# Kernel tuning notes

Measured on AMD Instinct MI355X. Metric: run time of the kernel, lower is better.

The kernel has to match this reference:

```python
import jax, jax.numpy as jnp
import numpy as np


def _build_kkt(A, B, x0, C, c, T):
    n_state, n_ctrl = B.shape
    n_all = n_state + n_ctrl
    N = n_all * T          # primal dim (z)
    M = n_state * T        # dual dim (mu)
    dt = A.dtype

    # TL = block_diag(C_0, ..., C_{T-1})  -> [N, N]
    t = jnp.arange(T)
    ra = jnp.arange(n_all)
    rows = t[:, None, None] * n_all + ra[None, :, None]
    cols = t[:, None, None] * n_all + ra[None, None, :]
    TL = jnp.zeros((N, N), dt).at[rows, cols].set(C)

    # BL = dynamics constraint matrix  -> [M, N]
    AB = jnp.concatenate([A, B], axis=1)            # [n_state, n_all]
    BL = jnp.zeros((M, N), dt)
    BL = BL.at[:n_state, :n_state].set(jnp.eye(n_state, dtype=dt))
    ti = jnp.arange(T - 1)
    rs = jnp.arange(n_state)
    # AB blocks: rows n_state + i*n_state, cols i*n_all (i = 0..T-2)
    br = (ti[:, None, None] + 1) * n_state + rs[None, :, None]
    bc = ti[:, None, None] * n_all + ra[None, None, :]
    BL = BL.at[br, bc].set(jnp.broadcast_to(AB, (T - 1, n_state, n_all)))
    # -1 identity blocks: BL[n_state*t + i, n_all*t + i] = -1 for t = 1..T-1
    BL = BL.at[(ti[:, None] + 1) * n_state + rs[None, :],
               (ti[:, None] + 1) * n_all + rs[None, :]].set(-1.0)

    Full = jnp.block([[TL, BL.T],
                      [BL, jnp.zeros((M, M), dt)]])
    b = jnp.zeros(M, dt).at[:n_state].set(x0)
    sol = jnp.concatenate([-c.reshape(-1), b])
    return Full, sol, N


def setup_inputs() -> dict:
    key = jax.random.key(0)
    kA, kB, kx, kC, kc = jax.random.split(key, 5)
    T, n_state, n_ctrl = 128, 16, 8
    n_all = n_state + n_ctrl
    A = 0.3 * jax.random.normal(kA, (n_state, n_state), jnp.float32)
    B = 0.3 * jax.random.normal(kB, (n_state, n_ctrl), jnp.float32)
    x0 = jax.random.normal(kx, (n_state,), jnp.float32)
    Mrand = 0.1 * jax.random.normal(kC, (T, n_all, n_all), jnp.float32)
    C = jnp.eye(n_all, dtype=jnp.float32)[None] + jnp.einsum('tij,tkj->tik', Mrand, Mrand)
    c = jax.random.normal(kc, (T, n_all), jnp.float32)
    return {"A": A, "B": B, "x0": x0, "C": C, "c": c, "T": T}


def reference(A, B, x0, C, c, T):
    Full, sol, N = _build_kkt(A, B, x0, C, c, T)
    mu_z = jnp.linalg.solve(Full, sol)
    z, mu = mu_z[:N], mu_z[N:]
    return (z, mu)
```

## Files before the change

### kernel.cpp

```cpp
#include <hip/hip_runtime.h>


constexpr int T  = 128;
constexpr int NA = 24;

__device__ __forceinline__ float dot16f4(const float* a, const float* b, float s) {
    const float4* a4 = (const float4*)a;
    const float4* b4 = (const float4*)b;
#pragma unroll
    for (int q = 0; q < 4; ++q) {
        float4 x = a4[q], y = b4[q];
        s = fmaf(x.x, y.x, s); s = fmaf(x.y, y.y, s);
        s = fmaf(x.z, y.z, s); s = fmaf(x.w, y.w, s);
    }
    return s;
}

__global__ __launch_bounds__(256, 1)
void lqr_solve(const float* __restrict__ gA,
               const float* __restrict__ gB,
               const float* __restrict__ gx0,
               const float* __restrict__ gC,
               const float* __restrict__ gc,
               float* __restrict__ out,
               float* __restrict__ Pws,
               float* __restrict__ pws)
{
    __shared__ __align__(16) float A_sh[16][16];
    __shared__ __align__(16) float At_sh[16][16];
    __shared__ __align__(16) float B_sh[16][8];
    __shared__ __align__(16) float Bt_sh[8][16];
    __shared__ __align__(16) float P_sh[2][16][20];
    __shared__ __align__(16) float p_sh[2][16];
    __shared__ __align__(16) float Wt[16][20];
    __shared__ __align__(16) float Vt[8][20];
    __shared__ __align__(16) float Gu[16][8];
    __shared__ __align__(16) float Aug[2][8][27];
    __shared__ __align__(16) float Kall[T][8][16];
    __shared__ __align__(16) float kall[T][8];
    __shared__ __align__(16) float c_sh[T][NA];
    __shared__ __align__(16) float z_sh[T][NA];
    __shared__ __align__(16) float Csh[2][24][25];

    const int tid = threadIdx.x;

    {
        const int i = tid >> 4, j = tid & 15;
        const float v = gA[tid];
        A_sh[i][j] = v; At_sh[j][i] = v;
        P_sh[0][i][j] = 0.0f;
        if (j < 4) P_sh[0][i][16 + j] = 0.0f;
    }
    if (tid < 128) {
        const int i = tid >> 3, j = tid & 7;
        const float v = gB[tid];
        B_sh[i][j] = v; Bt_sh[j][i] = v;
    }
    if (tid < 16) p_sh[0][tid] = 0.0f;
    for (int idx = tid; idx < T * NA; idx += 256) c_sh[idx / NA][idx % NA] = gc[idx];
    for (int idx = tid; idx < 576; idx += 256)
        Csh[0][idx / 24][idx % 24] = gC[(T - 1) * 576 + idx];
    __syncthreads();

    int pb = 0;
    for (int t = T - 1; t >= 0; --t) {
        const int cb = (T - 1 - t) & 1;

        float pf0 = 0.f, pf1 = 0.f, pf2 = 0.f;
        if (t > 0) {
            const float* src = gC + (size_t)(t - 1) * 576;
            pf0 = src[tid];
            pf1 = src[tid + 256];
            if (tid < 64) pf2 = src[tid + 512];
        }

        {
            const int j = tid >> 4, k = tid & 15;
            Wt[j][k] = dot16f4(&P_sh[pb][k][0], &At_sh[j][0], 0.0f);
            if (tid < 128) {
                const int jb = tid >> 4;
                Vt[jb][k] = dot16f4(&P_sh[pb][k][0], &Bt_sh[jb][0], 0.0f);
            }
        }
        __syncthreads();

        if (tid < 200) {
            const int i = tid / 25, j = tid % 25;
            float s;
            if (j < 8) {
                s = dot16f4(&Bt_sh[i][0], &Vt[j][0], Csh[cb][16 + i][16 + j]);
            } else if (j < 24) {
                const int jj = j - 8;
                s = dot16f4(&Bt_sh[i][0], &Wt[jj][0], Csh[cb][16 + i][jj]);
            } else {
                s = dot16f4(&Bt_sh[i][0], &p_sh[pb][0], c_sh[t][16 + i]);
            }
            Aug[0][i][j] = s;
        }
        if (tid < 128) {
            const int i = tid >> 3, j = tid & 7;
            Gu[i][j] = dot16f4(&At_sh[i][0], &Vt[j][0], Csh[cb][i][16 + j]);
        }
        __syncthreads();

        #pragma unroll
        for (int kk = 0; kk < 8; kk += 2) {
            const int rb = (kk >> 1) & 1, wb = rb ^ 1;
            if (tid < 200) {
                const int i = tid / 25, j = tid % 25;
                const float a  = Aug[rb][kk][kk],     b = Aug[rb][kk][kk + 1];
                const float c2 = Aug[rb][kk + 1][kk], d = Aug[rb][kk + 1][kk + 1];
                const float rdet = 1.0f / fmaf(a, d, -b * c2);
                const float pk0 = Aug[rb][kk][j], pk1 = Aug[rb][kk + 1][j];
                const float w0 = (d * pk0 - b * pk1) * rdet;
                const float w1 = (a * pk1 - c2 * pk0) * rdet;
                float v;
                if (i == kk)          v = w0;
                else if (i == kk + 1) v = w1;
                else v = fmaf(-Aug[rb][i][kk], w0,
                              fmaf(-Aug[rb][i][kk + 1], w1, Aug[rb][i][j]));
                Aug[wb][i][j] = v;
            }
            __syncthreads();
        }

        {
            const int i = tid >> 4, j = tid & 15;
            float s = dot16f4(&At_sh[i][0], &Wt[j][0], Csh[cb][i][j]);
            float s2 = 0.f;
            const float4 g0 = *(const float4*)&Gu[i][0];
            const float4 g1 = *(const float4*)&Gu[i][4];
            s2 = fmaf(g0.x, Aug[0][0][8 + j], s2);
            s2 = fmaf(g0.y, Aug[0][1][8 + j], s2);
            s2 = fmaf(g0.z, Aug[0][2][8 + j], s2);
            s2 = fmaf(g0.w, Aug[0][3][8 + j], s2);
            s2 = fmaf(g1.x, Aug[0][4][8 + j], s2);
            s2 = fmaf(g1.y, Aug[0][5][8 + j], s2);
            s2 = fmaf(g1.z, Aug[0][6][8 + j], s2);
            s2 = fmaf(g1.w, Aug[0][7][8 + j], s2);
            const float v = s - s2;
            P_sh[pb ^ 1][i][j] = v;
            Pws[t * 256 + tid] = v;
        }
        if (tid < 128) {
            const int i = tid >> 4, j = tid & 15;
            Kall[t][i][j] = Aug[0][i][8 + j];
        } else if (tid < 136) {
            kall[t][tid - 128] = Aug[0][tid - 128][24];
        }
        if (tid < 16) {
            float s = dot16f4(&At_sh[tid][0], &p_sh[pb][0], c_sh[t][tid]);
            float s2 = 0.f;
            #pragma unroll
            for (int q = 0; q < 8; ++q) s2 = fmaf(Gu[tid][q], Aug[0][q][24], s2);
            const float v = s - s2;
            p_sh[pb ^ 1][tid] = v;
            pws[t * 16 + tid] = v;
        }
        if (t > 0) {
            Csh[cb ^ 1][tid / 24][tid % 24] = pf0;
            Csh[cb ^ 1][(tid + 256) / 24][(tid + 256) % 24] = pf1;
            if (tid < 64) Csh[cb ^ 1][(tid + 512) / 24][(tid + 512) % 24] = pf2;
        }
        __syncthreads();
        pb ^= 1;
    }

    if (tid < 16) z_sh[0][tid] = gx0[tid];
    __syncthreads();
    for (int t = 0; t < T; ++t) {
        if (tid < 8) {
            float s = dot16f4(&Kall[t][tid][0], &z_sh[t][0], kall[t][tid]);
            z_sh[t][16 + tid] = -s;
        }
        if (tid >= 32 && tid < 48) {
            const int i = tid - 32;
            float s = pws[t * 16 + i];
            const float4* Pr = (const float4*)(Pws + t * 256 + i * 16);
            const float4* zr = (const float4*)&z_sh[t][0];
            #pragma unroll
            for (int q = 0; q < 4; ++q) {
                float4 p = Pr[q], z = zr[q];
                s = fmaf(p.x, z.x, s); s = fmaf(p.y, z.y, s);
                s = fmaf(p.z, z.z, s); s = fmaf(p.w, z.w, s);
            }
            if (t == 0) s = -s;
            out[T * NA + t * 16 + i] = s;
        }
        __syncthreads();
        if (t < T - 1 && tid < 16) {
            float s = dot16f4(&A_sh[tid][0], &z_sh[t][0], 0.0f);
            const float4 b0 = *(const float4*)&B_sh[tid][0];
            const float4 b1 = *(const float4*)&B_sh[tid][4];
            const float4 u0 = *(const float4*)&z_sh[t][16];
            const float4 u1 = *(const float4*)&z_sh[t][20];
            s = fmaf(b0.x, u0.x, s); s = fmaf(b0.y, u0.y, s);
            s = fmaf(b0.z, u0.z, s); s = fmaf(b0.w, u0.w, s);
            s = fmaf(b1.x, u1.x, s); s = fmaf(b1.y, u1.y, s);
            s = fmaf(b1.z, u1.z, s); s = fmaf(b1.w, u1.w, s);
            z_sh[t + 1][tid] = s;
        }
        __syncthreads();
    }

    for (int idx = tid; idx < T * NA; idx += 256)
        out[idx] = z_sh[idx / 24][idx % 24];
}

extern "C" void kernel_launch(void* const* d_in, const int* in_sizes, int n_in,
                              void* d_out, int out_size, void* d_ws, size_t ws_size,
                              hipStream_t stream) {
    const float* gA  = (const float*)d_in[0];
    const float* gB  = (const float*)d_in[1];
    const float* gx0 = (const float*)d_in[2];
    const float* gC  = (const float*)d_in[3];
    const float* gc  = (const float*)d_in[4];
    float* out = (float*)d_out;
    float* Pws = (float*)d_ws;
    float* pws = Pws + T * 256;
    lqr_solve<<<dim3(1), dim3(256), 0, stream>>>(gA, gB, gx0, gC, gc, out, Pws, pws);
}
```

Before: 408.2 us.

## Run LQR Riccati solve with a single 64-lane wavefront

Shrinks the block from 256 threads to one 64-wide wavefront and has each lane loop over several work items per stage. With one wave, __syncthreads barriers only need to wait on that wave, which is meant to cut the cost of the many per-step barriers in the serial backward recursion. The 2x2 pivot determinant is hoisted out of the per-item loop, and an explicit vmcnt wait is added before the forward pass so the global P/p writes are complete before they are read back. The trade-off is about four times the arithmetic per lane, which lengthens each step's critical path.

```diff
diff --git a/kernel.cpp b/kernel.cpp
--- a/kernel.cpp
+++ b/kernel.cpp
@@ -16,7 +16,7 @@
     return s;
 }
 
-__global__ __launch_bounds__(256, 1)
+__global__ __launch_bounds__(64, 1)
 void lqr_solve(const float* __restrict__ gA,
                const float* __restrict__ gB,
                const float* __restrict__ gx0,
@@ -42,23 +42,27 @@
     __shared__ __align__(16) float z_sh[T][NA];
     __shared__ __align__(16) float Csh[2][24][25];
 
-    const int tid = threadIdx.x;
-
-    {
-        const int i = tid >> 4, j = tid & 15;
-        const float v = gA[tid];
+    const int l = threadIdx.x;
+
+#pragma unroll
+    for (int r = 0; r < 4; ++r) {
+        const int u = l + 64 * r;
+        const int i = u >> 4, j = u & 15;
+        const float v = gA[u];
         A_sh[i][j] = v; At_sh[j][i] = v;
         P_sh[0][i][j] = 0.0f;
         if (j < 4) P_sh[0][i][16 + j] = 0.0f;
     }
-    if (tid < 128) {
-        const int i = tid >> 3, j = tid & 7;
-        const float v = gB[tid];
+#pragma unroll
+    for (int r = 0; r < 2; ++r) {
+        const int u = l + 64 * r;
+        const int i = u >> 3, j = u & 7;
+        const float v = gB[u];
         B_sh[i][j] = v; Bt_sh[j][i] = v;
     }
-    if (tid < 16) p_sh[0][tid] = 0.0f;
-    for (int idx = tid; idx < T * NA; idx += 256) c_sh[idx / NA][idx % NA] = gc[idx];
-    for (int idx = tid; idx < 576; idx += 256)
+    if (l < 16) p_sh[0][l] = 0.0f;
+    for (int idx = l; idx < T * NA; idx += 64) c_sh[idx / NA][idx % NA] = gc[idx];
+    for (int idx = l; idx < 576; idx += 64)
         Csh[0][idx / 24][idx % 24] = gC[(T - 1) * 576 + idx];
     __syncthreads();
 
@@ -66,39 +70,48 @@
     for (int t = T - 1; t >= 0; --t) {
         const int cb = (T - 1 - t) & 1;
 
-        float pf0 = 0.f, pf1 = 0.f, pf2 = 0.f;
+        float pf[9];
         if (t > 0) {
             const float* src = gC + (size_t)(t - 1) * 576;
-            pf0 = src[tid];
-            pf1 = src[tid + 256];
-            if (tid < 64) pf2 = src[tid + 512];
-        }
-
-        {
-            const int j = tid >> 4, k = tid & 15;
+#pragma unroll
+            for (int r = 0; r < 9; ++r) pf[r] = src[l + 64 * r];
+        }
+
+#pragma unroll
+        for (int r = 0; r < 4; ++r) {
+            const int u = l + 64 * r;
+            const int j = u >> 4, k = u & 15;
             Wt[j][k] = dot16f4(&P_sh[pb][k][0], &At_sh[j][0], 0.0f);
-            if (tid < 128) {
-                const int jb = tid >> 4;
-                Vt[jb][k] = dot16f4(&P_sh[pb][k][0], &Bt_sh[jb][0], 0.0f);
-            }
-        }
-        __syncthreads();
-
-        if (tid < 200) {
-            const int i = tid / 25, j = tid % 25;
-            float s;
-            if (j < 8) {
-                s = dot16f4(&Bt_sh[i][0], &Vt[j][0], Csh[cb][16 + i][16 + j]);
-            } else if (j < 24) {
-                const int jj = j - 8;
-                s = dot16f4(&Bt_sh[i][0], &Wt[jj][0], Csh[cb][16 + i][jj]);
-            } else {
-                s = dot16f4(&Bt_sh[i][0], &p_sh[pb][0], c_sh[t][16 + i]);
-            }
-            Aug[0][i][j] = s;
-        }
-        if (tid < 128) {
-            const int i = tid >> 3, j = tid & 7;
+        }
+#pragma unroll
+        for (int r = 0; r < 2; ++r) {
+            const int u = l + 64 * r;
+            const int jb = u >> 4, k = u & 15;
+            Vt[jb][k] = dot16f4(&P_sh[pb][k][0], &Bt_sh[jb][0], 0.0f);
+        }
+        __syncthreads();
+
+#pragma unroll
+        for (int r = 0; r < 4; ++r) {
+            const int u = l + 64 * r;
+            if (u < 200) {
+                const int i = u / 25, j = u % 25;
+                float s;
+                if (j < 8) {
+                    s = dot16f4(&Bt_sh[i][0], &Vt[j][0], Csh[cb][16 + i][16 + j]);
+                } else if (j < 24) {
+                    const int jj = j - 8;
+                    s = dot16f4(&Bt_sh[i][0], &Wt[jj][0], Csh[cb][16 + i][jj]);
+                } else {
+                    s = dot16f4(&Bt_sh[i][0], &p_sh[pb][0], c_sh[t][16 + i]);
+                }
+                Aug[0][i][j] = s;
+            }
+        }
+#pragma unroll
+        for (int r = 0; r < 2; ++r) {
+            const int u = l + 64 * r;
+            const int i = u >> 3, j = u & 7;
             Gu[i][j] = dot16f4(&At_sh[i][0], &Vt[j][0], Csh[cb][i][16 + j]);
         }
         __syncthreads();
@@ -106,26 +119,32 @@
         #pragma unroll
         for (int kk = 0; kk < 8; kk += 2) {
             const int rb = (kk >> 1) & 1, wb = rb ^ 1;
-            if (tid < 200) {
-                const int i = tid / 25, j = tid % 25;
-                const float a  = Aug[rb][kk][kk],     b = Aug[rb][kk][kk + 1];
-                const float c2 = Aug[rb][kk + 1][kk], d = Aug[rb][kk + 1][kk + 1];
-                const float rdet = 1.0f / fmaf(a, d, -b * c2);
-                const float pk0 = Aug[rb][kk][j], pk1 = Aug[rb][kk + 1][j];
-                const float w0 = (d * pk0 - b * pk1) * rdet;
-                const float w1 = (a * pk1 - c2 * pk0) * rdet;
-                float v;
-                if (i == kk)          v = w0;
-                else if (i == kk + 1) v = w1;
-                else v = fmaf(-Aug[rb][i][kk], w0,
-                              fmaf(-Aug[rb][i][kk + 1], w1, Aug[rb][i][j]));
-                Aug[wb][i][j] = v;
+            const float a  = Aug[rb][kk][kk],     b = Aug[rb][kk][kk + 1];
+            const float c2 = Aug[rb][kk + 1][kk], d = Aug[rb][kk + 1][kk + 1];
+            const float rdet = 1.0f / fmaf(a, d, -b * c2);
+#pragma unroll
+            for (int r = 0; r < 4; ++r) {
+                const int u = l + 64 * r;
+                if (u < 200) {
+                    const int i = u / 25, j = u % 25;
+                    const float pk0 = Aug[rb][kk][j], pk1 = Aug[rb][kk + 1][j];
+                    const float w0 = (d * pk0 - b * pk1) * rdet;
+                    const float w1 = (a * pk1 - c2 * pk0) * rdet;
+                    float v;
+                    if (i == kk)          v = w0;
+                    else if (i == kk + 1) v = w1;
+                    else v = fmaf(-Aug[rb][i][kk], w0,
+                                  fmaf(-Aug[rb][i][kk + 1], w1, Aug[rb][i][j]));
+                    Aug[wb][i][j] = v;
+                }
             }
             __syncthreads();
         }
 
-        {
-            const int i = tid >> 4, j = tid & 15;
+#pragma unroll
+        for (int r = 0; r < 4; ++r) {
+            const int u = l + 64 * r;
+            const int i = u >> 4, j = u & 15;
             float s = dot16f4(&At_sh[i][0], &Wt[j][0], Csh[cb][i][j]);
             float s2 = 0.f;
             const float4 g0 = *(const float4*)&Gu[i][0];
@@ -140,41 +159,46 @@
             s2 = fmaf(g1.w, Aug[0][7][8 + j], s2);
             const float v = s - s2;
             P_sh[pb ^ 1][i][j] = v;
-            Pws[t * 256 + tid] = v;
-        }
-        if (tid < 128) {
-            const int i = tid >> 4, j = tid & 15;
+            Pws[t * 256 + u] = v;
+        }
+#pragma unroll
+        for (int r = 0; r < 2; ++r) {
+            const int u = l + 64 * r;
+            const int i = u >> 4, j = u & 15;
             Kall[t][i][j] = Aug[0][i][8 + j];
-        } else if (tid < 136) {
-            kall[t][tid - 128] = Aug[0][tid - 128][24];
-        }
-        if (tid < 16) {
-            float s = dot16f4(&At_sh[tid][0], &p_sh[pb][0], c_sh[t][tid]);
+        }
+        if (l < 8) kall[t][l] = Aug[0][l][24];
+        if (l < 16) {
+            float s = dot16f4(&At_sh[l][0], &p_sh[pb][0], c_sh[t][l]);
             float s2 = 0.f;
             #pragma unroll
-            for (int q = 0; q < 8; ++q) s2 = fmaf(Gu[tid][q], Aug[0][q][24], s2);
+            for (int q = 0; q < 8; ++q) s2 = fmaf(Gu[l][q], Aug[0][q][24], s2);
             const float v = s - s2;
-            p_sh[pb ^ 1][tid] = v;
-            pws[t * 16 + tid] = v;
+            p_sh[pb ^ 1][l] = v;
+            pws[t * 16 + l] = v;
         }
         if (t > 0) {
-            Csh[cb ^ 1][tid / 24][tid % 24] = pf0;
-            Csh[cb ^ 1][(tid + 256) / 24][(tid + 256) % 24] = pf1;
-            if (tid < 64) Csh[cb ^ 1][(tid + 512) / 24][(tid + 512) % 24] = pf2;
+#pragma unroll
+            for (int r = 0; r < 9; ++r) {
+                const int u = l + 64 * r;
+                Csh[cb ^ 1][u / 24][u % 24] = pf[r];
+            }
         }
         __syncthreads();
         pb ^= 1;
     }
 
-    if (tid < 16) z_sh[0][tid] = gx0[tid];
+    asm volatile("s_waitcnt vmcnt(0)" ::: "memory");
+
+    if (l < 16) z_sh[0][l] = gx0[l];
     __syncthreads();
     for (int t = 0; t < T; ++t) {
-        if (tid < 8) {
-            float s = dot16f4(&Kall[t][tid][0], &z_sh[t][0], kall[t][tid]);
-            z_sh[t][16 + tid] = -s;
-        }
-        if (tid >= 32 && tid < 48) {
-            const int i = tid - 32;
+        if (l < 8) {
+            float s = dot16f4(&Kall[t][l][0], &z_sh[t][0], kall[t][l]);
+            z_sh[t][16 + l] = -s;
+        }
+        if (l >= 32 && l < 48) {
+            const int i = l - 32;
             float s = pws[t * 16 + i];
             const float4* Pr = (const float4*)(Pws + t * 256 + i * 16);
             const float4* zr = (const float4*)&z_sh[t][0];
@@ -188,22 +212,22 @@
             out[T * NA + t * 16 + i] = s;
         }
         __syncthreads();
-        if (t < T - 1 && tid < 16) {
-            float s = dot16f4(&A_sh[tid][0], &z_sh[t][0], 0.0f);
-            const float4 b0 = *(const float4*)&B_sh[tid][0];
-            const float4 b1 = *(const float4*)&B_sh[tid][4];
+        if (t < T - 1 && l < 16) {
+            float s = dot16f4(&A_sh[l][0], &z_sh[t][0], 0.0f);
+            const float4 b0 = *(const float4*)&B_sh[l][0];
+            const float4 b1 = *(const float4*)&B_sh[l][4];
             const float4 u0 = *(const float4*)&z_sh[t][16];
             const float4 u1 = *(const float4*)&z_sh[t][20];
             s = fmaf(b0.x, u0.x, s); s = fmaf(b0.y, u0.y, s);
             s = fmaf(b0.z, u0.z, s); s = fmaf(b0.w, u0.w, s);
             s = fmaf(b1.x, u1.x, s); s = fmaf(b1.y, u1.y, s);
             s = fmaf(b1.z, u1.z, s); s = fmaf(b1.w, u1.w, s);
-            z_sh[t + 1][tid] = s;
-        }
-        __syncthreads();
-    }
-
-    for (int idx = tid; idx < T * NA; idx += 256)
+            z_sh[t + 1][l] = s;
+        }
+        __syncthreads();
+    }
+
+    for (int idx = l; idx < T * NA; idx += 64)
         out[idx] = z_sh[idx / 24][idx % 24];
 }
 
@@ -218,5 +242,5 @@
     float* out = (float*)d_out;
     float* Pws = (float*)d_ws;
     float* pws = Pws + T * 256;
-    lqr_solve<<<dim3(1), dim3(256), 0, stream>>>(gA, gB, gx0, gC, gc, out, Pws, pws);
+    lqr_solve<<<dim3(1), dim3(64), 0, stream>>>(gA, gB, gx0, gC, gc, out, Pws, pws);
 }
```

Result: slower. 669.5 us (+64.0%).

## Fold closed-loop dynamics into backward pass, 4x4 block elimination, register-cached operands

Applied to the files above, without the earlier changes.

The backward Riccati sweep now precomputes the closed-loop matrix F=A-BK and offset d=-Bk per step and stores them in workspace. The forward rollout can then update the state with one matvec and one barrier per step, with the next step's F and P rows prefetched into registers. The 8x8 Gauss-Jordan elimination steps through 4x4 blocks (two barrier phases instead of four), writing K/k directly in the last phase. Loop-invariant rows of A^T and B^T are also cached in registers. The cost is extra global writes and more register pressure in the serial backward loop.

```diff
diff --git a/kernel.cpp b/kernel.cpp
--- a/kernel.cpp
+++ b/kernel.cpp
@@ -4,6 +4,16 @@
 constexpr int T  = 128;
 constexpr int NA = 24;
 
+__device__ __forceinline__ float dot16r(const float* lds, const float* r, float s) {
+    const float4* a4 = (const float4*)lds;
+#pragma unroll
+    for (int q = 0; q < 4; ++q) {
+        float4 x = a4[q];
+        s = fmaf(x.x, r[4 * q + 0], s); s = fmaf(x.y, r[4 * q + 1], s);
+        s = fmaf(x.z, r[4 * q + 2], s); s = fmaf(x.w, r[4 * q + 3], s);
+    }
+    return s;
+}
 __device__ __forceinline__ float dot16f4(const float* a, const float* b, float s) {
     const float4* a4 = (const float4*)a;
     const float4* b4 = (const float4*)b;
@@ -24,7 +34,9 @@
                const float* __restrict__ gc,
                float* __restrict__ out,
                float* __restrict__ Pws,
-               float* __restrict__ pws)
+               float* __restrict__ pws,
+               float* __restrict__ Fws,
+               float* __restrict__ dws)
 {
     __shared__ __align__(16) float A_sh[16][16];
     __shared__ __align__(16) float At_sh[16][16];
@@ -62,6 +74,35 @@
         Csh[0][idx / 24][idx % 24] = gC[(T - 1) * 576 + idx];
     __syncthreads();
 
+    float atr[16], btr_e[16], btr3[16], atr2[16], brow[8], browp[8];
+    {
+        const int rA  = tid >> 4;
+        const int rBe = (tid >> 4) & 7;
+        const int rB3 = (tid / 25) & 7;
+        const int rA2 = (tid >> 3) & 15;
+        const int rBp = tid & 15;
+#pragma unroll
+        for (int q = 0; q < 4; ++q) {
+            float4 v;
+            v = *(const float4*)&At_sh[rA][4 * q];
+            atr[4*q]=v.x; atr[4*q+1]=v.y; atr[4*q+2]=v.z; atr[4*q+3]=v.w;
+            v = *(const float4*)&Bt_sh[rBe][4 * q];
+            btr_e[4*q]=v.x; btr_e[4*q+1]=v.y; btr_e[4*q+2]=v.z; btr_e[4*q+3]=v.w;
+            v = *(const float4*)&Bt_sh[rB3][4 * q];
+            btr3[4*q]=v.x; btr3[4*q+1]=v.y; btr3[4*q+2]=v.z; btr3[4*q+3]=v.w;
+            v = *(const float4*)&At_sh[rA2][4 * q];
+            atr2[4*q]=v.x; atr2[4*q+1]=v.y; atr2[4*q+2]=v.z; atr2[4*q+3]=v.w;
+        }
+#pragma unroll
+        for (int q = 0; q < 2; ++q) {
+            float4 v;
+            v = *(const float4*)&B_sh[rA][4 * q];
+            brow[4*q]=v.x; brow[4*q+1]=v.y; brow[4*q+2]=v.z; brow[4*q+3]=v.w;
+            v = *(const float4*)&B_sh[rBp][4 * q];
+            browp[4*q]=v.x; browp[4*q+1]=v.y; browp[4*q+2]=v.z; browp[4*q+3]=v.w;
+        }
+    }
+
     int pb = 0;
     for (int t = T - 1; t >= 0; --t) {
         const int cb = (T - 1 - t) & 1;
@@ -76,10 +117,9 @@
 
         {
             const int j = tid >> 4, k = tid & 15;
-            Wt[j][k] = dot16f4(&P_sh[pb][k][0], &At_sh[j][0], 0.0f);
+            Wt[j][k] = dot16r(&P_sh[pb][k][0], atr, 0.0f);
             if (tid < 128) {
-                const int jb = tid >> 4;
-                Vt[jb][k] = dot16f4(&P_sh[pb][k][0], &Bt_sh[jb][0], 0.0f);
+                Vt[j][k] = dot16r(&P_sh[pb][k][0], btr_e, 0.0f);
             }
         }
         __syncthreads();
@@ -88,74 +128,113 @@
             const int i = tid / 25, j = tid % 25;
             float s;
             if (j < 8) {
-                s = dot16f4(&Bt_sh[i][0], &Vt[j][0], Csh[cb][16 + i][16 + j]);
+                s = dot16r(&Vt[j][0], btr3, Csh[cb][16 + i][16 + j]);
             } else if (j < 24) {
                 const int jj = j - 8;
-                s = dot16f4(&Bt_sh[i][0], &Wt[jj][0], Csh[cb][16 + i][jj]);
+                s = dot16r(&Wt[jj][0], btr3, Csh[cb][16 + i][jj]);
             } else {
-                s = dot16f4(&Bt_sh[i][0], &p_sh[pb][0], c_sh[t][16 + i]);
+                s = dot16r(&p_sh[pb][0], btr3, c_sh[t][16 + i]);
             }
             Aug[0][i][j] = s;
         }
         if (tid < 128) {
             const int i = tid >> 3, j = tid & 7;
-            Gu[i][j] = dot16f4(&At_sh[i][0], &Vt[j][0], Csh[cb][i][16 + j]);
+            Gu[i][j] = dot16r(&Vt[j][0], atr2, Csh[cb][i][16 + j]);
         }
         __syncthreads();
 
-        #pragma unroll
-        for (int kk = 0; kk < 8; kk += 2) {
-            const int rb = (kk >> 1) & 1, wb = rb ^ 1;
+#pragma unroll
+        for (int kk = 0; kk < 8; kk += 4) {
+            const int rb = (kk >> 2) & 1, wb = rb ^ 1;
+            const float m00=Aug[rb][kk+0][kk+0], m01=Aug[rb][kk+0][kk+1],
+                        m02=Aug[rb][kk+0][kk+2], m03=Aug[rb][kk+0][kk+3];
+            const float m10=Aug[rb][kk+1][kk+0], m11=Aug[rb][kk+1][kk+1],
+                        m12=Aug[rb][kk+1][kk+2], m13=Aug[rb][kk+1][kk+3];
+            const float m20=Aug[rb][kk+2][kk+0], m21=Aug[rb][kk+2][kk+1],
+                        m22=Aug[rb][kk+2][kk+2], m23=Aug[rb][kk+2][kk+3];
+            const float m30=Aug[rb][kk+3][kk+0], m31=Aug[rb][kk+3][kk+1],
+                        m32=Aug[rb][kk+3][kk+2], m33=Aug[rb][kk+3][kk+3];
+            const float ra   = 1.0f / fmaf(m00, m11, -m01 * m10);
+            const float ai00 =  m11 * ra, ai01 = -m01 * ra;
+            const float ai10 = -m10 * ra, ai11 =  m00 * ra;
+            const float aib00 = ai00*m02 + ai01*m12, aib01 = ai00*m03 + ai01*m13;
+            const float aib10 = ai10*m02 + ai11*m12, aib11 = ai10*m03 + ai11*m13;
+            const float s00 = m22 - (m20*aib00 + m21*aib10);
+            const float s01 = m23 - (m20*aib01 + m21*aib11);
+            const float s10 = m32 - (m30*aib00 + m31*aib10);
+            const float s11 = m33 - (m30*aib01 + m31*aib11);
+            const float rs   = 1.0f / fmaf(s00, s11, -s01 * s10);
+            const float si00 =  s11 * rs, si01 = -s01 * rs;
+            const float si10 = -s10 * rs, si11 =  s00 * rs;
             if (tid < 200) {
                 const int i = tid / 25, j = tid % 25;
-                const float a  = Aug[rb][kk][kk],     b = Aug[rb][kk][kk + 1];
-                const float c2 = Aug[rb][kk + 1][kk], d = Aug[rb][kk + 1][kk + 1];
-                const float rdet = 1.0f / fmaf(a, d, -b * c2);
-                const float pk0 = Aug[rb][kk][j], pk1 = Aug[rb][kk + 1][j];
-                const float w0 = (d * pk0 - b * pk1) * rdet;
-                const float w1 = (a * pk1 - c2 * pk0) * rdet;
+                const float pt0 = Aug[rb][kk+0][j], pt1 = Aug[rb][kk+1][j];
+                const float pq0 = Aug[rb][kk+2][j], pq1 = Aug[rb][kk+3][j];
+                const float y0 = ai00*pt0 + ai01*pt1;
+                const float y1 = ai10*pt0 + ai11*pt1;
+                const float z0 = pq0 - (m20*y0 + m21*y1);
+                const float z1 = pq1 - (m30*y0 + m31*y1);
+                const float w2 = si00*z0 + si01*z1;
+                const float w3 = si10*z0 + si11*z1;
+                const float w0 = y0 - (aib00*w2 + aib01*w3);
+                const float w1 = y1 - (aib10*w2 + aib11*w3);
                 float v;
-                if (i == kk)          v = w0;
+                if      (i == kk + 0) v = w0;
                 else if (i == kk + 1) v = w1;
-                else v = fmaf(-Aug[rb][i][kk], w0,
-                              fmaf(-Aug[rb][i][kk + 1], w1, Aug[rb][i][j]));
+                else if (i == kk + 2) v = w2;
+                else if (i == kk + 3) v = w3;
+                else {
+                    v = Aug[rb][i][j];
+                    v = fmaf(-Aug[rb][i][kk+0], w0, v);
+                    v = fmaf(-Aug[rb][i][kk+1], w1, v);
+                    v = fmaf(-Aug[rb][i][kk+2], w2, v);
+                    v = fmaf(-Aug[rb][i][kk+3], w3, v);
+                }
                 Aug[wb][i][j] = v;
+                if (kk == 4 && j >= 8) {
+                    if (j < 24) Kall[t][i][j - 8] = v;
+                    else        kall[t][i] = v;
+                }
             }
             __syncthreads();
         }
 
         {
             const int i = tid >> 4, j = tid & 15;
-            float s = dot16f4(&At_sh[i][0], &Wt[j][0], Csh[cb][i][j]);
+            float kc[8];
+#pragma unroll
+            for (int y = 0; y < 8; ++y) kc[y] = Aug[0][y][8 + j];
+            float s = dot16r(&Wt[j][0], atr, Csh[cb][i][j]);
             float s2 = 0.f;
             const float4 g0 = *(const float4*)&Gu[i][0];
             const float4 g1 = *(const float4*)&Gu[i][4];
-            s2 = fmaf(g0.x, Aug[0][0][8 + j], s2);
-            s2 = fmaf(g0.y, Aug[0][1][8 + j], s2);
-            s2 = fmaf(g0.z, Aug[0][2][8 + j], s2);
-            s2 = fmaf(g0.w, Aug[0][3][8 + j], s2);
-            s2 = fmaf(g1.x, Aug[0][4][8 + j], s2);
-            s2 = fmaf(g1.y, Aug[0][5][8 + j], s2);
-            s2 = fmaf(g1.z, Aug[0][6][8 + j], s2);
-            s2 = fmaf(g1.w, Aug[0][7][8 + j], s2);
+            s2 = fmaf(g0.x, kc[0], s2); s2 = fmaf(g0.y, kc[1], s2);
+            s2 = fmaf(g0.z, kc[2], s2); s2 = fmaf(g0.w, kc[3], s2);
+            s2 = fmaf(g1.x, kc[4], s2); s2 = fmaf(g1.y, kc[5], s2);
+            s2 = fmaf(g1.z, kc[6], s2); s2 = fmaf(g1.w, kc[7], s2);
             const float v = s - s2;
             P_sh[pb ^ 1][i][j] = v;
             Pws[t * 256 + tid] = v;
-        }
-        if (tid < 128) {
-            const int i = tid >> 4, j = tid & 15;
-            Kall[t][i][j] = Aug[0][i][8 + j];
-        } else if (tid < 136) {
-            kall[t][tid - 128] = Aug[0][tid - 128][24];
+            float fa = 0.f;
+#pragma unroll
+            for (int y = 0; y < 8; ++y) fa = fmaf(brow[y], kc[y], fa);
+            Fws[t * 256 + tid] = A_sh[i][j] - fa;
         }
         if (tid < 16) {
+            float kk8[8];
+#pragma unroll
+            for (int q = 0; q < 8; ++q) kk8[q] = Aug[0][q][24];
             float s = dot16f4(&At_sh[tid][0], &p_sh[pb][0], c_sh[t][tid]);
             float s2 = 0.f;
-            #pragma unroll
-            for (int q = 0; q < 8; ++q) s2 = fmaf(Gu[tid][q], Aug[0][q][24], s2);
+#pragma unroll
+            for (int q = 0; q < 8; ++q) s2 = fmaf(Gu[tid][q], kk8[q], s2);
             const float v = s - s2;
             p_sh[pb ^ 1][tid] = v;
             pws[t * 16 + tid] = v;
+            float da = 0.f;
+#pragma unroll
+            for (int y = 0; y < 8; ++y) da = fmaf(browp[y], kk8[y], da);
+            dws[t * 16 + tid] = -da;
         }
         if (t > 0) {
             Csh[cb ^ 1][tid / 24][tid % 24] = pf0;
@@ -166,41 +245,91 @@
         pb ^= 1;
     }
 
+    asm volatile("s_waitcnt vmcnt(0)" ::: "memory");
+
     if (tid < 16) z_sh[0][tid] = gx0[tid];
+    float fcur[16], dcur = 0.f, prow[16], pcur = 0.f;
+    if (tid < 16) {
+#pragma unroll
+        for (int q = 0; q < 4; ++q) {
+            float4 v = *(const float4*)&Fws[tid * 16 + 4 * q];
+            fcur[4*q]=v.x; fcur[4*q+1]=v.y; fcur[4*q+2]=v.z; fcur[4*q+3]=v.w;
+        }
+        dcur = dws[tid];
+    }
+    if (tid >= 32 && tid < 48) {
+        const int i = tid - 32;
+#pragma unroll
+        for (int q = 0; q < 4; ++q) {
+            float4 v = *(const float4*)&Pws[i * 16 + 4 * q];
+            prow[4*q]=v.x; prow[4*q+1]=v.y; prow[4*q+2]=v.z; prow[4*q+3]=v.w;
+        }
+        pcur = pws[i];
+    }
     __syncthreads();
     for (int t = 0; t < T; ++t) {
-        if (tid < 8) {
-            float s = dot16f4(&Kall[t][tid][0], &z_sh[t][0], kall[t][tid]);
-            z_sh[t][16 + tid] = -s;
+        float fn[16], dn = 0.f, pn[16], ppn = 0.f;
+        if (t < T - 1) {
+            if (tid < 16) {
+#pragma unroll
+                for (int q = 0; q < 4; ++q) {
+                    float4 v = *(const float4*)&Fws[(t + 1) * 256 + tid * 16 + 4 * q];
+                    fn[4*q]=v.x; fn[4*q+1]=v.y; fn[4*q+2]=v.z; fn[4*q+3]=v.w;
+                }
+                dn = dws[(t + 1) * 16 + tid];
+            }
+            if (tid >= 32 && tid < 48) {
+                const int i = tid - 32;
+#pragma unroll
+                for (int q = 0; q < 4; ++q) {
+                    float4 v = *(const float4*)&Pws[(t + 1) * 256 + i * 16 + 4 * q];
+                    pn[4*q]=v.x; pn[4*q+1]=v.y; pn[4*q+2]=v.z; pn[4*q+3]=v.w;
+                }
+                ppn = pws[(t + 1) * 16 + i];
+            }
+        }
+        if (tid >= 16 && tid < 24) {
+            const int y = tid - 16;
+            float s = dot16f4(&Kall[t][y][0], &z_sh[t][0], kall[t][y]);
+            z_sh[t][16 + y] = -s;
         }
         if (tid >= 32 && tid < 48) {
             const int i = tid - 32;
-            float s = pws[t * 16 + i];
-            const float4* Pr = (const float4*)(Pws + t * 256 + i * 16);
+            float s = pcur;
             const float4* zr = (const float4*)&z_sh[t][0];
-            #pragma unroll
+#pragma unroll
             for (int q = 0; q < 4; ++q) {
-                float4 p = Pr[q], z = zr[q];
-                s = fmaf(p.x, z.x, s); s = fmaf(p.y, z.y, s);
-                s = fmaf(p.z, z.z, s); s = fmaf(p.w, z.w, s);
+                float4 z = zr[q];
+                s = fmaf(prow[4*q+0], z.x, s); s = fmaf(prow[4*q+1], z.y, s);
+                s = fmaf(prow[4*q+2], z.z, s); s = fmaf(prow[4*q+3], z.w, s);
             }
             if (t == 0) s = -s;
             out[T * NA + t * 16 + i] = s;
         }
+        if (t < T - 1 && tid < 16) {
+            const float4* zr = (const float4*)&z_sh[t][0];
+            float s = dcur;
+#pragma unroll
+            for (int q = 0; q < 4; ++q) {
+                float4 z = zr[q];
+                s = fmaf(fcur[4*q+0], z.x, s); s = fmaf(fcur[4*q+1], z.y, s);
+                s = fmaf(fcur[4*q+2], z.z, s); s = fmaf(fcur[4*q+3], z.w, s);
+            }
+            z_sh[t + 1][tid] = s;
+        }
         __syncthreads();
-        if (t < T - 1 && tid < 16) {
-            float s = dot16f4(&A_sh[tid][0], &z_sh[t][0], 0.0f);
-            const float4 b0 = *(const float4*)&B_sh[tid][0];
-            const float4 b1 = *(const float4*)&B_sh[tid][4];
-            const float4 u0 = *(const float4*)&z_sh[t][16];
-            const float4 u1 = *(const float4*)&z_sh[t][20];
-            s = fmaf(b0.x, u0.x, s); s = fmaf(b0.y, u0.y, s);
-            s = fmaf(b0.z, u0.z, s); s = fmaf(b0.w, u0.w, s);
-            s = fmaf(b1.x, u1.x, s); s = fmaf(b1.y, u1.y, s);
-            s = fmaf(b1.z, u1.z, s); s = fmaf(b1.w, u1.w, s);
-            z_sh[t + 1][tid] = s;
-        }
-        __syncthreads();
+        if (t < T - 1) {
+            if (tid < 16) {
+#pragma unroll
+                for (int q = 0; q < 16; ++q) fcur[q] = fn[q];
+                dcur = dn;
+            }
+            if (tid >= 32 && tid < 48) {
+#pragma unroll
+                for (int q = 0; q < 16; ++q) prow[q] = pn[q];
+                pcur = ppn;
+            }
+        }
     }
 
     for (int idx = tid; idx < T * NA; idx += 256)
@@ -218,5 +347,8 @@
     float* out = (float*)d_out;
     float* Pws = (float*)d_ws;
     float* pws = Pws + T * 256;
-    lqr_solve<<<dim3(1), dim3(256), 0, stream>>>(gA, gB, gx0, gC, gc, out, Pws, pws);
+    float* Fws = pws + T * 16;
+    float* dws = Fws + T * 256;
+    lqr_solve<<<dim3(1), dim3(256), 0, stream>>>(gA, gB, gx0, gC, gc, out,
+                                                 Pws, pws, Fws, dws);
 }
```

After: 366.5 us. 10.2% less time.
